# Kernel optimization log

Measured on AMD Instinct MI355X. Metric: run time of the kernel, lower is better.

## Reference

```python
import jax, jax.numpy as jnp
import numpy as np

BS = 32  # leaf block size
NUM_HOPS = 1  # ATTENTION_HOPS


def setup_inputs() -> dict:
    key = jax.random.key(0)
    ks = jax.random.split(key, 10)
    B, N, C, H = 1, 131072, 256, 4
    E = 8 * N
    x = jax.random.normal(ks[0], (B, N, C), dtype=jnp.float32)
    rows = jax.random.randint(ks[1], (E,), 0, N)
    offs = jax.random.randint(ks[2], (E,), 0, BS)
    cols = (rows // BS) * BS + offs  # in-block neighbors
    edge_index = jnp.stack([rows, cols]).astype(jnp.int64)
    edge_values = jax.random.normal(ks[3], (E,), dtype=jnp.float32)
    positions = jax.random.uniform(ks[4], (N, 3), dtype=jnp.float32)
    qkv_w = jax.random.normal(ks[5], (3 * C, C), dtype=jnp.float32) * 0.02
    qkv_b = jnp.zeros((3 * C,), dtype=jnp.float32)
    proj_w = jax.random.normal(ks[6], (C, C), dtype=jnp.float32) * 0.02
    proj_b = jnp.zeros((C,), dtype=jnp.float32)
    gate_w = jax.random.normal(ks[7], (H, 4), dtype=jnp.float32) * 0.01  # init std=0.01
    gate_b = jnp.zeros((H,), dtype=jnp.float32)
    return {"x": x, "edge_index": edge_index, "edge_values": edge_values,
            "positions": positions, "qkv_w": qkv_w, "qkv_b": qkv_b,
            "proj_w": proj_w, "proj_b": proj_b, "gate_w": gate_w, "gate_b": gate_b}


def _connectivity(edge_index, edge_values, positions, nb):
    rows, cols = edge_index[0], edge_index[1]
    br, bc = rows // BS, cols // BS
    in_block = (br == bc) & (br < nb)
    r_l, c_l = rows % BS, cols % BS
    b_safe = jnp.where(in_block, br, nb)  # out-of-range -> dropped by scatter
    dx = positions[cols] - positions[rows]            # [E,3]
    ef_flat = jnp.concatenate([dx, edge_values[:, None]], axis=1)  # [E,4]
    adj = jnp.zeros((nb, BS, BS), jnp.float32).at[b_safe, r_l, c_l].set(1.0, mode='drop')
    eye = jnp.eye(BS, dtype=jnp.float32)
    reachable = jnp.broadcast_to(eye[None], (nb, BS, BS))
    cur = adj
    for _ in range(NUM_HOPS):
        reachable = jnp.clip(reachable + cur, 0.0, 1.0)
        cur = jnp.matmul(cur, adj)
    attn_mask = jnp.concatenate([reachable, jnp.ones((nb, BS, 1), jnp.float32)], axis=2)
    edge_feats = jnp.zeros((nb, BS, BS + 1, 4), jnp.float32)
    edge_feats = edge_feats.at[b_safe, r_l, c_l, :].set(ef_flat, mode='drop')
    return attn_mask, edge_feats


def reference(x, edge_index, edge_values, positions, qkv_w, qkv_b, proj_w, proj_b, gate_w, gate_b):
    B, N, C = x.shape
    H = gate_w.shape[0]
    hd = C // H
    scale = hd ** -0.5
    nb = N // BS  # N chosen divisible by BS (no pad)
    attn_mask, edge_feats = _connectivity(edge_index, edge_values, positions, nb)

    x_blk = x.reshape(B, nb, BS, C)
    block_node = x_blk.mean(axis=2, keepdims=True)
    kv = jnp.concatenate([x_blk, block_node], axis=2)  # [B,nb,BS+1,C]
    qkv_q = x_blk @ qkv_w.T + qkv_b
    qkv_kv = kv @ qkv_w.T + qkv_b
    q = qkv_q[..., :C].reshape(B, nb, BS, H, hd)
    k = qkv_kv[..., C:2 * C].reshape(B, nb, BS + 1, H, hd)
    v = qkv_kv[..., 2 * C:].reshape(B, nb, BS + 1, H, hd)

    scores = jnp.einsum('bnqhd,bnkhd->bnqkh', q, k) * scale

    ar = jnp.arange(BS)
    bias_physics = edge_feats.at[:, :, BS, :].set(0.0).at[:, :, BS, 3].set(1.0)
    bias_physics = bias_physics.at[:, ar, ar, :].set(0.0).at[:, ar, ar, 3].set(1.0)

    scores = scores + bias_physics[None, ..., 3:4]
    mask = attn_mask[None, :, :, :, None]  # [1,nb,BS,BS+1,1]
    scores = jnp.where(mask == 0, -jnp.inf, scores)
    attn_probs = jax.nn.softmax(scores, axis=3)

    gate = bias_physics @ gate_w.T + gate_b  # [nb,BS,BS+1,H]
    gate = jnp.where(mask == 0, 0.0, gate[None])
    combined = attn_probs + gate

    x_out = jnp.einsum('bnqkh,bnkhd->bnqhd', combined, v).reshape(B, nb, BS, C)
    out = x_out.reshape(B, N, C) @ proj_w.T + proj_b
    return out
```

## Files before the change

### kernel.cpp

```cpp
#include <hip/hip_runtime.h>
#include <math.h>

#define BSZ 32
#define CH  256

typedef short  bf16x8 __attribute__((ext_vector_type(8)));
typedef float  f32x4  __attribute__((ext_vector_type(4)));
typedef unsigned short ushort_t;
typedef unsigned int   uint_t;

#define MFMA(a, b, c) __builtin_amdgcn_mfma_f32_16x16x32_bf16((a), (b), (c), 0, 0, 0)

__device__ __forceinline__ ushort_t f2b(float f) {
    uint_t u = __builtin_bit_cast(uint_t, f);
    uint_t r = (u + 0x7FFFu + ((u >> 16) & 1u)) >> 16;
    return (ushort_t)r;
}
__device__ __forceinline__ float b2f(ushort_t u) {
    uint_t v = ((uint_t)u) << 16;
    return __builtin_bit_cast(float, v);
}
__device__ __forceinline__ uint_t pk2(float a, float b) {
    return (uint_t)f2b(a) | ((uint_t)f2b(b) << 16);
}

__global__ void edge_win_kernel(const int* __restrict__ ei, int E, int nb,
                                int* __restrict__ win) {
    int e = blockIdx.x * blockDim.x + threadIdx.x;
    if (e >= E) return;
    int r = ei[e];
    int c = ei[E + e];
    int br = r >> 5, bc = c >> 5;
    if (br == bc && br < nb) {
        atomicMax(&win[br * (BSZ * BSZ) + (r & 31) * BSZ + (c & 31)], e);
    }
}

__global__ void edge_feat_kernel(const int* __restrict__ ei,
                                 const float* __restrict__ ev,
                                 const float* __restrict__ pos,
                                 const int* __restrict__ win, int E,
                                 ushort_t* __restrict__ cellinfo,
                                 uint_t* __restrict__ vmap) {
    int e = blockIdx.x * blockDim.x + threadIdx.x;
    if (e >= E) return;
    int r = ei[e];
    int c = ei[E + e];
    int br = r >> 5, bc = c >> 5;
    if (br != bc) return;
    int rl = r & 31, cl = c & 31;
    int cell = br * 1024 + rl * 32 + cl;
    if (win[cell] != e) return;
    float d0 = pos[c * 3 + 0] - pos[r * 3 + 0];
    float d1 = pos[c * 3 + 1] - pos[r * 3 + 1];
    float d2 = pos[c * 3 + 2] - pos[r * 3 + 2];
    float d3 = ev[e];
    uint2 w; w.x = pk2(d0, d1); w.y = pk2(d2, d3);
    *(uint2*)&cellinfo[(size_t)cell * 4] = w;
    atomicOr(&vmap[br * 32 + rl], 1u << cl);
}

__global__ void wconv_kernel(const float* __restrict__ qkv_w,
                             const float* __restrict__ proj_w,
                             ushort_t* __restrict__ qkv_wf,
                             ushort_t* __restrict__ proj_wf) {
    int i = blockIdx.x * blockDim.x + threadIdx.x;
    int lane = i & 63, ks = (i >> 6) & 7, tile = i >> 9;
    int l15 = lane & 15, lg = lane >> 4;
    if (tile < 48) {
        const float* src = qkv_w + (size_t)(tile * 16 + l15) * 256 + ks * 32 + lg * 8;
        ushort_t* dst = qkv_wf + (size_t)i * 8;
        #pragma unroll
        for (int e = 0; e < 8; ++e) dst[e] = f2b(src[e]);
    }
    if (tile < 16) {
        const float* src = proj_w + (size_t)(tile * 16 + l15) * 256 + ks * 32 + lg * 8;
        ushort_t* dst = proj_wf + (size_t)i * 8;
        #pragma unroll
        for (int e = 0; e < 8; ++e) dst[e] = f2b(src[e]);
    }
}

#define LS_XB   0
#define LS_QS   32768
#define LS_KS   65536
#define LS_VS   98304
#define LS_TOT  131072

__global__ __launch_bounds__(512, 2)
void fused_attn(const float* __restrict__ x,
                const ushort_t* __restrict__ qkv_wf,
                const float* __restrict__ qkv_b,
                const ushort_t* __restrict__ cellinfo,
                const uint_t* __restrict__ vmap,
                const ushort_t* __restrict__ proj_wf,
                const float* __restrict__ proj_b,
                const float* __restrict__ gate_w,
                const float* __restrict__ gate_b,
                float* __restrict__ out)
{
    __shared__ __align__(16) char smem[LS_TOT];
    ushort_t* xb   = (ushort_t*)(smem + LS_XB);
    ushort_t* comb = (ushort_t*)(smem + LS_XB);
    ushort_t* qs   = (ushort_t*)(smem + LS_QS);
    ushort_t* xo   = (ushort_t*)(smem + LS_QS);
    ushort_t* ksm  = (ushort_t*)(smem + LS_KS);
    ushort_t* vs   = (ushort_t*)(smem + LS_VS);

    const int t = threadIdx.x;
    const int w = t >> 6, lane = t & 63, l15 = lane & 15, lg = lane >> 4;
    const int bi = blockIdx.x;
    const int mbase = bi * 64;

    #pragma unroll
    for (int i = 0; i < 8; ++i) {
        int flat = i * 2048 + t * 4;
        int r = flat >> 8, c = flat & 255;
        float4 xv = *(const float4*)&x[(size_t)(mbase + r) * CH + c];
        uint2 wv; wv.x = pk2(xv.x, xv.y); wv.y = pk2(xv.z, xv.w);
        *(uint2*)&xb[r * 256 + (c ^ ((r & 7) << 3))] = wv;
    }
    __syncthreads();

    const int slB = (l15 & 7) << 3;
    const f32x4 zf = {0.f, 0.f, 0.f, 0.f};

    bf16x8 xf[8][4];
    #pragma unroll
    for (int ks = 0; ks < 8; ++ks) {
        int k0 = (ks * 32 + lg * 8) ^ slB;
        xf[ks][0] = *(const bf16x8*)&xb[l15 * 256 + k0];
        xf[ks][1] = *(const bf16x8*)&xb[(16 + l15) * 256 + k0];
        xf[ks][2] = *(const bf16x8*)&xb[(32 + l15) * 256 + k0];
        xf[ks][3] = *(const bf16x8*)&xb[(48 + l15) * 256 + k0];
    }

    bf16x8 wA[8], wB[8];

#define LOADT(dst, itv) { _Pragma("unroll")                                   \
        for (int ks_ = 0; ks_ < 8; ++ks_)                                     \
            dst[ks_] = *(const bf16x8*)(qkv_wf                                \
                + ((size_t)((((itv) * 8 + w) * 8) + ks_)) * 512 + lane * 8); }

#define TILE_COMPUTE(CUR, SW) { _Pragma("unroll")                             \
        for (int ks_ = 0; ks_ < 8; ++ks_) {                                   \
            if (SW) {                                                         \
                a0 = MFMA(CUR[ks_], xf[ks_][0], a0);                          \
                a1 = MFMA(CUR[ks_], xf[ks_][1], a1);                          \
                a2 = MFMA(CUR[ks_], xf[ks_][2], a2);                          \
                a3 = MFMA(CUR[ks_], xf[ks_][3], a3);                          \
            } else {                                                          \
                a0 = MFMA(xf[ks_][0], CUR[ks_], a0);                          \
                a1 = MFMA(xf[ks_][1], CUR[ks_], a1);                          \
                a2 = MFMA(xf[ks_][2], CUR[ks_], a2);                          \
                a3 = MFMA(xf[ks_][3], CUR[ks_], a3);                          \
            } } }

#define STORE_QK(ITV) {                                                       \
        int tt_ = (ITV) * 8 + w;                                              \
        f32x4 bv4_ = *(const f32x4*)&qkv_b[tt_ * 16 + lg * 4];                \
        ushort_t* dst_ = ((ITV) < 2) ? qs : ksm;                              \
        int tloc_ = ((ITV) < 2) ? tt_ : tt_ - 16;                             \
        f32x4 av_[4] = {a0, a1, a2, a3};                                      \
        _Pragma("unroll")                                                     \
        for (int m_ = 0; m_ < 4; ++m_) {                                      \
            f32x4 v_ = av_[m_] + bv4_;                                        \
            uint2 wv_; wv_.x = pk2(v_[0], v_[1]); wv_.y = pk2(v_[2], v_[3]);  \
            *(uint2*)&dst_[(m_ >> 1) * 8192 + (tloc_ * 2 + (m_ & 1)) * 256    \
                           + lane * 4] = wv_;                                 \
        } }

#define STORE_V(ITV) {                                                        \
        int tt_ = (ITV) * 8 + w;                                              \
        int vch_ = (tt_ - 32) * 16 + l15;                                     \
        float bv_ = qkv_b[512 + vch_];                                        \
        int swzv_ = (vch_ & 3) << 3;                                          \
        f32x4 av_[4] = {a0, a1, a2, a3};                                      \
        _Pragma("unroll")                                                     \
        for (int m_ = 0; m_ < 4; ++m_) {                                      \
            f32x4 v_ = av_[m_];                                               \
            uint2 wv_; wv_.x = pk2(v_[0] + bv_, v_[1] + bv_);                 \
            wv_.y = pk2(v_[2] + bv_, v_[3] + bv_);                            \
            int roff_ = (((m_ & 1) * 16 + lg * 4)) ^ swzv_;                   \
            *(uint2*)&vs[(m_ >> 1) * 8192 + vch_ * 32 + roff_] = wv_;         \
        } }

#define DO_TILE(ITV, CUR) {                                                   \
        f32x4 a0 = zf, a1 = zf, a2 = zf, a3 = zf;                             \
        if ((ITV) < 4) { TILE_COMPUTE(CUR, 1) STORE_QK(ITV) }                 \
        else           { TILE_COMPUTE(CUR, 0) STORE_V(ITV) } }

    LOADT(wA, 0); LOADT(wB, 1);
    DO_TILE(0, wA); LOADT(wA, 2);
    DO_TILE(1, wB); LOADT(wB, 3);
    DO_TILE(2, wA); LOADT(wA, 4);
    DO_TILE(3, wB); LOADT(wB, 5);
    DO_TILE(4, wA);
    DO_TILE(5, wB);

    const int gl = w >> 2, h = w & 3;
    const ushort_t* crow = cellinfo + (size_t)(bi * 2 + gl) * 4096;
    uint4 cellA[2][2], cellB[2][2];
    uint_t vmq[2];
    #pragma unroll
    for (int qt = 0; qt < 2; ++qt) {
        int qi = qt * 16 + l15;
        vmq[qt] = vmap[(size_t)(bi * 2 + gl) * 32 + qi];
        #pragma unroll
        for (int kt = 0; kt < 2; ++kt) {
            int kj0 = kt * 16 + lg * 4;
            const uint_t* cp = (const uint_t*)(crow + ((size_t)qi * 32 + kj0) * 4);
            cellA[qt][kt] = *(const uint4*)cp;
            cellB[qt][kt] = *(const uint4*)(cp + 4);
        }
    }
    const float gw0 = gate_w[h * 4 + 0], gw1 = gate_w[h * 4 + 1];
    const float gw2 = gate_w[h * 4 + 2], gw3 = gate_w[h * 4 + 3];
    const float gb  = gate_b[h];

    __syncthreads();

    uint4 qld[2][2], kld[2][2];
    #pragma unroll
    for (int rt = 0; rt < 2; ++rt) {
        #pragma unroll
        for (int ks2 = 0; ks2 < 2; ++ks2) {
            int ttq = h * 4 + ks2 * 2 + (lg >> 1);
            int a0 = gl * 8192 + (ttq * 2 + rt) * 256 + ((lg & 1) * 32 + l15) * 4;
            uint2 u0 = *(const uint2*)&qs[a0];
            uint2 u1 = *(const uint2*)&qs[a0 + 64];
            qld[rt][ks2] = (uint4){u0.x, u0.y, u1.x, u1.y};
            uint2 w0 = *(const uint2*)&ksm[a0];
            uint2 w1 = *(const uint2*)&ksm[a0 + 64];
            kld[rt][ks2] = (uint4){w0.x, w0.y, w1.x, w1.y};
        }
    }
    bf16x8 vf[4];
    #pragma unroll
    for (int ct = 0; ct < 4; ++ct) {
        int off = (lg * 8) ^ ((l15 & 3) << 3);
        vf[ct] = *(const bf16x8*)&vs[gl * 8192
                                     + (h * 64 + ct * 16 + l15) * 32 + off];
    }
    __syncthreads();

    f32x4 s[2][2];
    #pragma unroll
    for (int qt = 0; qt < 2; ++qt) { s[qt][0] = zf; s[qt][1] = zf; }
    #pragma unroll
    for (int qt = 0; qt < 2; ++qt) {
        #pragma unroll
        for (int ks2 = 0; ks2 < 2; ++ks2) {
            bf16x8 qf = __builtin_bit_cast(bf16x8, qld[qt][ks2]);
            #pragma unroll
            for (int kt = 0; kt < 2; ++kt)
                s[qt][kt] = MFMA(__builtin_bit_cast(bf16x8, kld[kt][ks2]),
                                 qf, s[qt][kt]);
        }
    }

    #pragma unroll
    for (int qt = 0; qt < 2; ++qt) {
        int qi = qt * 16 + l15;
        float r[8], gt[8];
        float rawsum = 0.f;
        #pragma unroll
        for (int kt = 0; kt < 2; ++kt) {
            int kj0 = kt * 16 + lg * 4;
            uint4 cA = cellA[qt][kt], cB = cellB[qt][kt];
            uint_t d01[4] = {cA.x, cA.z, cB.x, cB.z};
            uint_t d23[4] = {cA.y, cA.w, cB.y, cB.w};
            #pragma unroll
            for (int j = 0; j < 4; ++j) {
                int kj = kj0 + j;
                bool fixed = (kj == qi);
                bool validb = (vmq[qt] >> kj) & 1u;
                float e3 = b2f((ushort_t)(d23[j] >> 16));
                float sb = fixed ? 1.0f : (validb ? e3 : -INFINITY);
                float g;
                if (fixed)       g = gw3 + gb;
                else if (validb) g = b2f((ushort_t)(d01[j] & 0xFFFF)) * gw0
                                   + b2f((ushort_t)(d01[j] >> 16))    * gw1
                                   + b2f((ushort_t)(d23[j] & 0xFFFF)) * gw2
                                   + e3 * gw3 + gb;
                else             g = 0.0f;
                float sraw = s[qt][kt][j];
                rawsum += sraw;
                r[kt * 4 + j]  = sraw * 0.125f + sb;
                gt[kt * 4 + j] = g;
            }
        }
        rawsum += __shfl_xor(rawsum, 16);
        rawsum += __shfl_xor(rawsum, 32);
        float r2 = rawsum * (0.125f / 32.0f) + 1.0f;

        float m = fmaxf(fmaxf(fmaxf(r[0], r[1]), fmaxf(r[2], r[3])),
                        fmaxf(fmaxf(r[4], r[5]), fmaxf(r[6], r[7])));
        m = fmaxf(m, r2);
        m = fmaxf(m, __shfl_xor(m, 16));
        m = fmaxf(m, __shfl_xor(m, 32));
        float sum = 0.f;
        #pragma unroll
        for (int i = 0; i < 8; ++i) { r[i] = __expf(r[i] - m); sum += r[i]; }
        sum += __shfl_xor(sum, 16);
        sum += __shfl_xor(sum, 32);
        float e2 = __expf(r2 - m);
        float inv = 1.0f / (sum + e2);
        float comb32 = e2 * inv + (gw3 + gb);
        float cadd = comb32 * 0.03125f;
        int swz = (l15 & 3) << 3;
        #pragma unroll
        for (int kt = 0; kt < 2; ++kt) {
            int kj0 = kt * 16 + lg * 4;
            uint2 wv;
            wv.x = pk2(r[kt*4+0] * inv + gt[kt*4+0] + cadd,
                       r[kt*4+1] * inv + gt[kt*4+1] + cadd);
            wv.y = pk2(r[kt*4+2] * inv + gt[kt*4+2] + cadd,
                       r[kt*4+3] * inv + gt[kt*4+3] + cadd);
            *(uint2*)&comb[(gl * 4 + h) * 1024 + qi * 32 + (kj0 ^ swz)] = wv;
        }
    }

    bf16x8 cfr[2];
    #pragma unroll
    for (int qt = 0; qt < 2; ++qt) {
        int qi = qt * 16 + l15;
        int off = (lg * 8) ^ ((l15 & 3) << 3);
        cfr[qt] = *(const bf16x8*)&comb[(gl * 4 + h) * 1024 + qi * 32 + off];
    }
    #pragma unroll
    for (int ct = 0; ct < 4; ++ct) {
        #pragma unroll
        for (int qt = 0; qt < 2; ++qt) {
            f32x4 acc2 = zf;
            acc2 = MFMA(vf[ct], cfr[qt], acc2);
            int qi = qt * 16 + l15;
            uint2 wv;
            wv.x = pk2(acc2[0], acc2[1]);
            wv.y = pk2(acc2[2], acc2[3]);
            int c0 = h * 64 + ct * 16 + lg * 4;
            *(uint2*)&xo[gl * 8192 + qi * 256 + (c0 ^ ((l15 & 7) << 3))] = wv;
        }
    }
    __syncthreads();

    {
        const int slR = (l15 & 7) << 3;
        bf16x8 pw[2][8];
        #pragma unroll
        for (int i = 0; i < 2; ++i) {
            int pt = w * 2 + i;
            #pragma unroll
            for (int ks = 0; ks < 8; ++ks)
                pw[i][ks] = *(const bf16x8*)(proj_wf
                               + ((size_t)(pt * 8 + ks)) * 512 + lane * 8);
        }
        f32x4 pacc[2][4];
        #pragma unroll
        for (int i = 0; i < 2; ++i)
            #pragma unroll
            for (int rt = 0; rt < 4; ++rt) pacc[i][rt] = zf;
        #pragma unroll
        for (int ks = 0; ks < 8; ++ks) {
            int k0 = ks * 32 + lg * 8;
            #pragma unroll
            for (int rt = 0; rt < 4; ++rt) {
                bf16x8 bfr = *(const bf16x8*)&xo[(rt >> 1) * 8192
                                 + ((rt & 1) * 16 + l15) * 256 + (k0 ^ slR)];
                pacc[0][rt] = MFMA(pw[0][ks], bfr, pacc[0][rt]);
                pacc[1][rt] = MFMA(pw[1][ks], bfr, pacc[1][rt]);
            }
        }
        #pragma unroll
        for (int i = 0; i < 2; ++i) {
            int pt = w * 2 + i, n0 = pt * 16;
            f32x4 bv = *(const f32x4*)&proj_b[n0 + lg * 4];
            #pragma unroll
            for (int rt = 0; rt < 4; ++rt) {
                f32x4 o = pacc[i][rt] + bv;
                int row = mbase + (rt >> 1) * 32 + (rt & 1) * 16 + l15;
                *(f32x4*)&out[(size_t)row * 256 + n0 + lg * 4] = o;
            }
        }
    }
}

extern "C" void kernel_launch(void* const* d_in, const int* in_sizes, int n_in,
                              void* d_out, int out_size, void* d_ws, size_t ws_size,
                              hipStream_t stream) {
    const float* x      = (const float*)d_in[0];
    const int*   ei     = (const int*)  d_in[1];
    const float* ev     = (const float*)d_in[2];
    const float* pos    = (const float*)d_in[3];
    const float* qkv_w  = (const float*)d_in[4];
    const float* qkv_b  = (const float*)d_in[5];
    const float* proj_w = (const float*)d_in[6];
    const float* proj_b = (const float*)d_in[7];
    const float* gate_w = (const float*)d_in[8];
    const float* gate_b = (const float*)d_in[9];
    float* out = (float*)d_out;

    const int E  = in_sizes[2];
    const int N  = in_sizes[0] / CH;
    const int nb = N / BSZ;

    char* ws = (char*)d_ws;
    int*      win      = (int*)ws;
    uint_t*   vmap     = (uint_t*)(ws + (size_t)nb * 4096);
    ushort_t* cellinfo = (ushort_t*)(ws + (size_t)nb * 4224);
    size_t off = (size_t)nb * 12416;
    ushort_t* qkv_wf  = (ushort_t*)(ws + off); off += 48 * 8 * 64 * 8 * 2;
    ushort_t* proj_wf = (ushort_t*)(ws + off); off += 16 * 8 * 64 * 8 * 2;

    hipMemsetAsync(win, 0xFF, (size_t)nb * 4096, stream);
    hipMemsetAsync(vmap, 0x00, (size_t)nb * 128, stream);
    edge_win_kernel<<<(E + 255) / 256, 256, 0, stream>>>(ei, E, nb, win);
    edge_feat_kernel<<<(E + 255) / 256, 256, 0, stream>>>(ei, ev, pos, win, E,
                                                          cellinfo, vmap);
    wconv_kernel<<<96, 256, 0, stream>>>(qkv_w, proj_w, qkv_wf, proj_wf);
    fused_attn<<<nb / 2, 512, 0, stream>>>(x, qkv_wf, qkv_b, cellinfo, vmap,
                                           proj_wf, proj_b, gate_w, gate_b, out);
}
```

Before: 269.6 us.

## Replace per-edge feature scatter with per-node position-gate projection and winner lookup

```diff
diff --git a/kernel.cpp b/kernel.cpp
--- a/kernel.cpp
+++ b/kernel.cpp
@@ -36,28 +36,15 @@
     }
 }
 
-__global__ void edge_feat_kernel(const int* __restrict__ ei,
-                                 const float* __restrict__ ev,
-                                 const float* __restrict__ pos,
-                                 const int* __restrict__ win, int E,
-                                 ushort_t* __restrict__ cellinfo,
-                                 uint_t* __restrict__ vmap) {
-    int e = blockIdx.x * blockDim.x + threadIdx.x;
-    if (e >= E) return;
-    int r = ei[e];
-    int c = ei[E + e];
-    int br = r >> 5, bc = c >> 5;
-    if (br != bc) return;
-    int rl = r & 31, cl = c & 31;
-    int cell = br * 1024 + rl * 32 + cl;
-    if (win[cell] != e) return;
-    float d0 = pos[c * 3 + 0] - pos[r * 3 + 0];
-    float d1 = pos[c * 3 + 1] - pos[r * 3 + 1];
-    float d2 = pos[c * 3 + 2] - pos[r * 3 + 2];
-    float d3 = ev[e];
-    uint2 w; w.x = pk2(d0, d1); w.y = pk2(d2, d3);
-    *(uint2*)&cellinfo[(size_t)cell * 4] = w;
-    atomicOr(&vmap[br * 32 + rl], 1u << cl);
+__global__ void pgate_kernel(const float* __restrict__ pos,
+                             const float* __restrict__ gate_w,
+                             float* __restrict__ pg, int N) {
+    int n = blockIdx.x * 256 + threadIdx.x;
+    int h = blockIdx.y;
+    if (n >= N) return;
+    pg[(size_t)h * N + n] = pos[n * 3 + 0] * gate_w[h * 4 + 0]
+                          + pos[n * 3 + 1] * gate_w[h * 4 + 1]
+                          + pos[n * 3 + 2] * gate_w[h * 4 + 2];
 }
 
 __global__ void wconv_kernel(const float* __restrict__ qkv_w,
@@ -91,13 +78,14 @@
 void fused_attn(const float* __restrict__ x,
                 const ushort_t* __restrict__ qkv_wf,
                 const float* __restrict__ qkv_b,
-                const ushort_t* __restrict__ cellinfo,
-                const uint_t* __restrict__ vmap,
+                const int* __restrict__ win,
+                const float* __restrict__ ev,
+                const float* __restrict__ pg,
                 const ushort_t* __restrict__ proj_wf,
                 const float* __restrict__ proj_b,
                 const float* __restrict__ gate_w,
                 const float* __restrict__ gate_b,
-                float* __restrict__ out)
+                float* __restrict__ out, int N)
 {
     __shared__ __align__(16) char smem[LS_TOT];
     ushort_t* xb   = (ushort_t*)(smem + LS_XB);
@@ -199,26 +187,39 @@
     DO_TILE(5, wB);
 
     const int gl = w >> 2, h = w & 3;
-    const ushort_t* crow = cellinfo + (size_t)(bi * 2 + gl) * 4096;
-    uint4 cellA[2][2], cellB[2][2];
-    uint_t vmq[2];
+    const int cb = mbase + gl * 32;
+    uint4  wv4[2][2];
+    float4 pgc[2];
+    float  pgr[2];
     #pragma unroll
     for (int qt = 0; qt < 2; ++qt) {
         int qi = qt * 16 + l15;
-        vmq[qt] = vmap[(size_t)(bi * 2 + gl) * 32 + qi];
+        wv4[qt][0] = *(const uint4*)&win[(size_t)(bi * 2 + gl) * 1024
+                                         + qi * 32 + lg * 4];
+        wv4[qt][1] = *(const uint4*)&win[(size_t)(bi * 2 + gl) * 1024
+                                         + qi * 32 + 16 + lg * 4];
+        pgr[qt] = pg[(size_t)h * N + cb + qi];
+    }
+    pgc[0] = *(const float4*)&pg[(size_t)h * N + cb + lg * 4];
+    pgc[1] = *(const float4*)&pg[(size_t)h * N + cb + 16 + lg * 4];
+    const float gw3v = gate_w[h * 4 + 3];
+    const float gbv  = gate_b[h];
+    const float g3b  = gw3v + gbv;
+
+    __syncthreads();
+
+    float evv[2][8];
+    #pragma unroll
+    for (int qt = 0; qt < 2; ++qt)
         #pragma unroll
         for (int kt = 0; kt < 2; ++kt) {
-            int kj0 = kt * 16 + lg * 4;
-            const uint_t* cp = (const uint_t*)(crow + ((size_t)qi * 32 + kj0) * 4);
-            cellA[qt][kt] = *(const uint4*)cp;
-            cellB[qt][kt] = *(const uint4*)(cp + 4);
-        }
-    }
-    const float gw0 = gate_w[h * 4 + 0], gw1 = gate_w[h * 4 + 1];
-    const float gw2 = gate_w[h * 4 + 2], gw3 = gate_w[h * 4 + 3];
-    const float gb  = gate_b[h];
-
-    __syncthreads();
+            const int* wp = (const int*)&wv4[qt][kt];
+            #pragma unroll
+            for (int j = 0; j < 4; ++j) {
+                int e = wp[j];
+                evv[qt][kt * 4 + j] = ev[e < 0 ? 0 : e];
+            }
+        }
 
     uint4 qld[2][2], kld[2][2];
     #pragma unroll
@@ -266,24 +267,17 @@
         float rawsum = 0.f;
         #pragma unroll
         for (int kt = 0; kt < 2; ++kt) {
-            int kj0 = kt * 16 + lg * 4;
-            uint4 cA = cellA[qt][kt], cB = cellB[qt][kt];
-            uint_t d01[4] = {cA.x, cA.z, cB.x, cB.z};
-            uint_t d23[4] = {cA.y, cA.w, cB.y, cB.w};
+            const int* wp = (const int*)&wv4[qt][kt];
             #pragma unroll
             for (int j = 0; j < 4; ++j) {
-                int kj = kj0 + j;
+                int kj = kt * 16 + lg * 4 + j;
                 bool fixed = (kj == qi);
-                bool validb = (vmq[qt] >> kj) & 1u;
-                float e3 = b2f((ushort_t)(d23[j] >> 16));
-                float sb = fixed ? 1.0f : (validb ? e3 : -INFINITY);
-                float g;
-                if (fixed)       g = gw3 + gb;
-                else if (validb) g = b2f((ushort_t)(d01[j] & 0xFFFF)) * gw0
-                                   + b2f((ushort_t)(d01[j] >> 16))    * gw1
-                                   + b2f((ushort_t)(d23[j] & 0xFFFF)) * gw2
-                                   + e3 * gw3 + gb;
-                else             g = 0.0f;
+                bool valid = wp[j] >= 0;
+                float e3 = evv[qt][kt * 4 + j];
+                float sb = fixed ? 1.0f : (valid ? e3 : -INFINITY);
+                float pgcv = ((const float*)&pgc[kt])[j];
+                float g = fixed ? g3b
+                        : (valid ? (pgcv - pgr[qt] + e3 * gw3v + gbv) : 0.0f);
                 float sraw = s[qt][kt][j];
                 rawsum += sraw;
                 r[kt * 4 + j]  = sraw * 0.125f + sb;
@@ -306,7 +300,7 @@
         sum += __shfl_xor(sum, 32);
         float e2 = __expf(r2 - m);
         float inv = 1.0f / (sum + e2);
-        float comb32 = e2 * inv + (gw3 + gb);
+        float comb32 = e2 * inv + g3b;
         float cadd = comb32 * 0.03125f;
         int swz = (l15 & 3) << 3;
         #pragma unroll
@@ -405,19 +399,17 @@
     const int nb = N / BSZ;
 
     char* ws = (char*)d_ws;
-    int*      win      = (int*)ws;
-    uint_t*   vmap     = (uint_t*)(ws + (size_t)nb * 4096);
-    ushort_t* cellinfo = (ushort_t*)(ws + (size_t)nb * 4224);
-    size_t off = (size_t)nb * 12416;
+    int*   win = (int*)ws;
+    float* pg  = (float*)(ws + (size_t)nb * 4096);
+    size_t off = (size_t)nb * 4096 + (size_t)4 * N * 4;
     ushort_t* qkv_wf  = (ushort_t*)(ws + off); off += 48 * 8 * 64 * 8 * 2;
     ushort_t* proj_wf = (ushort_t*)(ws + off); off += 16 * 8 * 64 * 8 * 2;
 
     hipMemsetAsync(win, 0xFF, (size_t)nb * 4096, stream);
-    hipMemsetAsync(vmap, 0x00, (size_t)nb * 128, stream);
     edge_win_kernel<<<(E + 255) / 256, 256, 0, stream>>>(ei, E, nb, win);
-    edge_feat_kernel<<<(E + 255) / 256, 256, 0, stream>>>(ei, ev, pos, win, E,
-                                                          cellinfo, vmap);
+    pgate_kernel<<<dim3((N + 255) / 256, 4), 256, 0, stream>>>(pos, gate_w, pg, N);
     wconv_kernel<<<96, 256, 0, stream>>>(qkv_w, proj_w, qkv_wf, proj_wf);
-    fused_attn<<<nb / 2, 512, 0, stream>>>(x, qkv_wf, qkv_b, cellinfo, vmap,
-                                           proj_wf, proj_b, gate_w, gate_b, out);
-}
+    fused_attn<<<nb / 2, 512, 0, stream>>>(x, qkv_wf, qkv_b, win, ev, pg,
+                                           proj_wf, proj_b, gate_w, gate_b,
+                                           out, N);
+}
```

Result: faster. 241.3 us (-10.5%).
